# Kernel optimization log

Measured on AMD Instinct MI355X. Metric: run time of the kernel, lower is better.

## Reference

```python
import jax, jax.numpy as jnp
import numpy as np

B, L, H, O, NL = 1024, 100, 256, 256, 2


def setup_inputs() -> dict:
    key = jax.random.key(0)
    ks = jax.random.split(key, 20)
    s = 0.05  # weight scale to keep gates/softmax well-conditioned
    d = {
        "encoder_outputs": jax.random.normal(ks[0], (B, L, H), jnp.float32),
        "enc_h": jax.random.normal(ks[1], (NL, B, H), jnp.float32),
        "enc_c": jax.random.normal(ks[2], (NL, B, H), jnp.float32),
        "embedding": jax.random.uniform(ks[3], (O, H), jnp.float32, -1.0, 1.0),
        # torch nn.LSTM params, gate order (i, f, g, o)
        "Wih0": jax.random.normal(ks[4], (4 * H, 2 * H), jnp.float32) * s,
        "Whh0": jax.random.normal(ks[5], (4 * H, H), jnp.float32) * s,
        "bih0": jax.random.normal(ks[6], (4 * H,), jnp.float32) * s,
        "bhh0": jax.random.normal(ks[7], (4 * H,), jnp.float32) * s,
        "Wih1": jax.random.normal(ks[8], (4 * H, H), jnp.float32) * s,
        "Whh1": jax.random.normal(ks[9], (4 * H, H), jnp.float32) * s,
        "bih1": jax.random.normal(ks[10], (4 * H,), jnp.float32) * s,
        "bhh1": jax.random.normal(ks[11], (4 * H,), jnp.float32) * s,
        "Wa": jax.random.normal(ks[12], (H, H), jnp.float32) * s,        # Luong general score
        "Wconcat": jax.random.normal(ks[13], (H, 2 * H), jnp.float32) * s,
        "Wout": jax.random.normal(ks[14], (O, H), jnp.float32) * s,
        "Wcrit": jax.random.normal(ks[15], (O, O), jnp.float32) * s,
        "bcrit": jax.random.normal(ks[16], (O,), jnp.float32) * s,
        "actions": jax.random.randint(ks[17], (B, L), 0, O, jnp.int32),
    }
    return d


def _lstm_cell(x, h, c, Wih, Whh, bih, bhh):
    gates = x @ Wih.T + h @ Whh.T + bih + bhh  # [B, 4H]
    i, f, g, o = jnp.split(gates, 4, axis=-1)
    i = jax.nn.sigmoid(i)
    f = jax.nn.sigmoid(f)
    g = jnp.tanh(g)
    o = jax.nn.sigmoid(o)
    c_new = f * c + i * g
    h_new = o * jnp.tanh(c_new)
    return h_new, c_new


def reference(encoder_outputs, enc_h, enc_c, embedding,
              Wih0, Whh0, bih0, bhh0, Wih1, Whh1, bih1, bhh1,
              Wa, Wconcat, Wout, Wcrit, bcrit, actions):
    # Precompute Luong 'general' projection of encoder states (same math each step)
    enc_proj = encoder_outputs @ Wa.T  # [B, L, H]

    def step(carry, act_t):
        x, h, c, ctx = carry  # x:[B] int, h/c:[NL,B,H], ctx:[B,H]
        emb = embedding[x]                               # [B, H]
        inp = jnp.concatenate([emb, ctx], axis=-1)       # [B, 2H]
        h0, c0 = _lstm_cell(inp, h[0], c[0], Wih0, Whh0, bih0, bhh0)
        h1, c1 = _lstm_cell(h0, h[1], c[1], Wih1, Whh1, bih1, bhh1)
        out = h1                                         # [B, H]
        scores = jnp.einsum('bh,blh->bl', out, enc_proj)  # Luong general score
        attn = jax.nn.softmax(scores, axis=-1)
        ctx_att = jnp.einsum('bl,blh->bh', attn, encoder_outputs)
        new_ctx = jnp.tanh(jnp.concatenate([out, ctx_att], axis=-1) @ Wconcat.T)  # [B, H]
        logit_raw = new_ctx @ Wout.T                     # [B, O]
        pi = jax.nn.softmax(logit_raw, axis=-1)
        Q = logit_raw @ Wcrit.T + bcrit
        new_carry = (act_t, jnp.stack([h0, h1]), jnp.stack([c0, c1]), new_ctx)
        return new_carry, (pi, Q)

    x0 = jnp.zeros((B,), jnp.int32)
    ctx0 = encoder_outputs.mean(axis=1)                  # [B, H]
    _, (pis, Qs) = jax.lax.scan(step, (x0, enc_h, enc_c, ctx0), actions.T)
    logits = jnp.transpose(pis, (1, 0, 2))               # [B, L, O] (softmax probs, as in torch code)
    qvalues = jnp.transpose(Qs, (1, 0, 2))               # [B, L, O]
    values = (qvalues * logits).sum(-1)                  # [B, L]
    decoder_action = actions.astype(jnp.float32)         # teacher-forced actions recorded per step
    return decoder_action, logits, values
```

## Files before the change

### kernel.cpp

```cpp
#include <hip/hip_runtime.h>


#define Bx 1024
#define Lq 100
#define Hd 256
#define Od 256
#define H4 1024

typedef _Float16 f16;
typedef _Float16 half2_t __attribute__((ext_vector_type(2)));
typedef _Float16 f16x4 __attribute__((ext_vector_type(4)));
typedef unsigned int uint;
typedef uint uint4v __attribute__((ext_vector_type(4)));

__device__ __forceinline__ float fdot2(half2_t a, half2_t b, float c) {
#if __has_builtin(__builtin_amdgcn_fdot2)
  return __builtin_amdgcn_fdot2(a, b, c, false);
#else
  return c + (float)a.x * (float)b.x + (float)a.y * (float)b.y;
#endif
}
__device__ __forceinline__ float dot8(float acc, float4 w, float4 a) {
  acc = fdot2(__builtin_bit_cast(half2_t, w.x), __builtin_bit_cast(half2_t, a.x), acc);
  acc = fdot2(__builtin_bit_cast(half2_t, w.y), __builtin_bit_cast(half2_t, a.y), acc);
  acc = fdot2(__builtin_bit_cast(half2_t, w.z), __builtin_bit_cast(half2_t, a.z), acc);
  acc = fdot2(__builtin_bit_cast(half2_t, w.w), __builtin_bit_cast(half2_t, a.w), acc);
  return acc;
}
__device__ __forceinline__ float sigmf(float x) { return 1.0f / (1.0f + __expf(-x)); }



__global__ void k_cvt_lstm(const float* Wih0, const float* Whh0,
                           const float* Wih1, const float* Whh1, f16* dst) {
  int row = blockIdx.x, seg = row >> 10, r = row & 1023, c = threadIdx.x;
  const float* src; int stride, off;
  if (seg == 0)      { src = Wih0; stride = 512; off = 256; }
  else if (seg == 1) { src = Whh0; stride = 256; off = 0; }
  else if (seg == 2) { src = Wih1; stride = 256; off = 0; }
  else               { src = Whh1; stride = 256; off = 0; }
  size_t didx = (size_t)seg * 262144 + (size_t)(r >> 6) * 16384 +
                (size_t)(c >> 3) * 512 + (size_t)(r & 63) * 8 + (c & 7);
  dst[didx] = (f16)src[(size_t)r * stride + off + c];
}

__global__ void k_cvt_small(const float* Wconcat, const float* Wout,
                            const float* Wcrit, const float* Wa, f16* dst) {
  int blk = blockIdx.x, seg = blk >> 8, r = blk & 255, c = threadIdx.x;
  if (seg == 0) {
    dst[(size_t)(r >> 6) * 32768 + (size_t)(c >> 3) * 512 + (r & 63) * 8 + (c & 7)] =
        (f16)Wconcat[(size_t)r * 512 + c];
    int c2 = c + 256;
    dst[(size_t)(r >> 6) * 32768 + (size_t)(c2 >> 3) * 512 + (r & 63) * 8 + (c2 & 7)] =
        (f16)Wconcat[(size_t)r * 512 + c2];
  } else if (seg == 1) {
    dst[131072 + (size_t)(r >> 6) * 16384 + (size_t)(c >> 3) * 512 + (r & 63) * 8 + (c & 7)] =
        (f16)Wout[(size_t)r * 256 + c];
  } else if (seg == 2) {
    dst[196608 + (size_t)(r >> 6) * 16384 + (size_t)(c >> 3) * 512 + (r & 63) * 8 + (c & 7)] =
        (f16)Wcrit[(size_t)r * 256 + c];
  } else {
    dst[262144 + (size_t)(c >> 6) * 16384 + (size_t)(r >> 3) * 512 + (c & 63) * 8 + (r & 7)] =
        (f16)Wa[(size_t)r * 256 + c];
  }
}

__global__ void k_bias1(const float* bih1, const float* bhh1, float* b1) {
  int i = blockIdx.x * 256 + threadIdx.x;
  b1[i] = bih1[i] + bhh1[i];
}

__global__ void k_actions(const int* actions, float* out) {
  int i = blockIdx.x * 256 + threadIdx.x;
  out[i] = (float)actions[i];
}

__global__ void k_cvt_enc(const float* enc, f16* dst) {
  size_t i = (size_t)blockIdx.x * 256 + threadIdx.x;
  const float4* s = (const float4*)enc;
  float4 v = s[i];
  f16x4 o = {(f16)v.x, (f16)v.y, (f16)v.z, (f16)v.w};
  *(f16x4*)(dst + 4 * i) = o;
}

__global__ void k_table0(const float* emb, const float* Wih0,
                         const float* bih0, const float* bhh0, float* t0) {
  __shared__ float shw[16][256];
  int j0 = blockIdx.x * 16, tid = threadIdx.x;
  for (int i = tid; i < 16 * 256; i += 256) {
    int r = i >> 8, c = i & 255;
    shw[r][c] = Wih0[(size_t)(j0 + r) * 512 + c];
  }
  __syncthreads();
  int a = tid;
  float acc[16];
#pragma unroll
  for (int r = 0; r < 16; r++) acc[r] = 0.f;
  for (int k = 0; k < 256; k++) {
    float e = emb[(size_t)a * 256 + k];
#pragma unroll
    for (int r = 0; r < 16; r++) acc[r] = fmaf(e, shw[r][k], acc[r]);
  }
#pragma unroll
  for (int r = 0; r < 16; r++)
    t0[(size_t)a * H4 + j0 + r] = acc[r] + bih0[j0 + r] + bhh0[j0 + r];
}

template <bool E16>
__launch_bounds__(1024)
__global__ void k_seq(const float* enc, const f16* enc16,
                      const float* enc_h, const float* enc_c,
                      const int* actions, const float* bcrit,
                      const f16* wWih0c, const f16* wWhh0,
                      const f16* wWih1, const f16* wWhh1,
                      const f16* wWconcat, const f16* wWout, const f16* wWcrit,
                      const f16* wWaT,
                      const float* table0, const float* bias1, float* out) {
  const int tid = threadIdx.x;
  const int b0 = blockIdx.x * 4;

  __shared__ _Float16 sh_h0[4][264];
  __shared__ _Float16 sh_h1[4][264];
  __shared__ _Float16 sh_ctx[4][264];
  __shared__ _Float16 sh_ca[4][264];
  __shared__ _Float16 sh_logit[4][264];
  __shared__ _Float16 sh_v[4][264];
  __shared__ float sh_c0[4][256];
  __shared__ float sh_c1[4][256];
  __shared__ float sh_gates[4][H4];
  __shared__ float sh_sc[4][128];
  __shared__ float sh_pi[4][256];
  __shared__ float sh_red[4][20];

  {
    int bb = tid >> 8, h = tid & 255, gb = b0 + bb;
    sh_h0[bb][h] = (f16)enc_h[(size_t)(0 * Bx + gb) * Hd + h];
    sh_h1[bb][h] = (f16)enc_h[(size_t)(1 * Bx + gb) * Hd + h];
    sh_c0[bb][h] = enc_c[(size_t)(0 * Bx + gb) * Hd + h];
    sh_c1[bb][h] = enc_c[(size_t)(1 * Bx + gb) * Hd + h];
    const float* ep = enc + (size_t)gb * Lq * Hd + h;
    float s = 0.f;
#pragma unroll 4
    for (int l = 0; l < Lq; l++) s += __builtin_nontemporal_load(ep + (size_t)l * Hd);
    sh_ctx[bb][h] = (f16)(s * (1.0f / Lq));
  }
  __syncthreads();

  for (int t = 0; t < Lq; t++) {
    {
      const int j = tid;
      const f16* w1 = wWih0c + (size_t)(j >> 6) * 16384 + (j & 63) * 8;
      const f16* w2 = wWhh0 + (size_t)(j >> 6) * 16384 + (j & 63) * 8;
      int ia0 = (t == 0) ? 0 : actions[(size_t)(b0 + 0) * Lq + (t - 1)];
      int ia1 = (t == 0) ? 0 : actions[(size_t)(b0 + 1) * Lq + (t - 1)];
      int ia2 = (t == 0) ? 0 : actions[(size_t)(b0 + 2) * Lq + (t - 1)];
      int ia3 = (t == 0) ? 0 : actions[(size_t)(b0 + 3) * Lq + (t - 1)];
      float a0 = table0[(size_t)ia0 * H4 + j];
      float a1 = table0[(size_t)ia1 * H4 + j];
      float a2 = table0[(size_t)ia2 * H4 + j];
      float a3 = table0[(size_t)ia3 * H4 + j];
#pragma unroll 4
      for (int c = 0; c < 32; c++) {
        float4 wa = *(const float4*)(w1 + (size_t)c * 512);
        float4 wb = *(const float4*)(w2 + (size_t)c * 512);
        float4 x0 = *(const float4*)&sh_ctx[0][8 * c];
        float4 x1 = *(const float4*)&sh_ctx[1][8 * c];
        float4 x2 = *(const float4*)&sh_ctx[2][8 * c];
        float4 x3 = *(const float4*)&sh_ctx[3][8 * c];
        a0 = dot8(a0, wa, x0); a1 = dot8(a1, wa, x1);
        a2 = dot8(a2, wa, x2); a3 = dot8(a3, wa, x3);
        float4 y0 = *(const float4*)&sh_h0[0][8 * c];
        float4 y1 = *(const float4*)&sh_h0[1][8 * c];
        float4 y2 = *(const float4*)&sh_h0[2][8 * c];
        float4 y3 = *(const float4*)&sh_h0[3][8 * c];
        a0 = dot8(a0, wb, y0); a1 = dot8(a1, wb, y1);
        a2 = dot8(a2, wb, y2); a3 = dot8(a3, wb, y3);
      }
      sh_gates[0][j] = a0; sh_gates[1][j] = a1;
      sh_gates[2][j] = a2; sh_gates[3][j] = a3;
    }
    __syncthreads();

    {
      int bb = tid >> 8, h = tid & 255;
      float gi = sh_gates[bb][h], gf = sh_gates[bb][h + 256];
      float gg = sh_gates[bb][h + 512], go = sh_gates[bb][h + 768];
      float c = sigmf(gf) * sh_c0[bb][h] + sigmf(gi) * tanhf(gg);
      sh_c0[bb][h] = c;
      sh_h0[bb][h] = (f16)(sigmf(go) * tanhf(c));
    }
    __syncthreads();

    {
      const int j = tid;
      const f16* w1 = wWih1 + (size_t)(j >> 6) * 16384 + (j & 63) * 8;
      const f16* w2 = wWhh1 + (size_t)(j >> 6) * 16384 + (j & 63) * 8;
      float bv = bias1[j];
      float a0 = bv, a1 = bv, a2 = bv, a3 = bv;
#pragma unroll 4
      for (int c = 0; c < 32; c++) {
        float4 wa = *(const float4*)(w1 + (size_t)c * 512);
        float4 wb = *(const float4*)(w2 + (size_t)c * 512);
        float4 x0 = *(const float4*)&sh_h0[0][8 * c];
        float4 x1 = *(const float4*)&sh_h0[1][8 * c];
        float4 x2 = *(const float4*)&sh_h0[2][8 * c];
        float4 x3 = *(const float4*)&sh_h0[3][8 * c];
        a0 = dot8(a0, wa, x0); a1 = dot8(a1, wa, x1);
        a2 = dot8(a2, wa, x2); a3 = dot8(a3, wa, x3);
        float4 y0 = *(const float4*)&sh_h1[0][8 * c];
        float4 y1 = *(const float4*)&sh_h1[1][8 * c];
        float4 y2 = *(const float4*)&sh_h1[2][8 * c];
        float4 y3 = *(const float4*)&sh_h1[3][8 * c];
        a0 = dot8(a0, wb, y0); a1 = dot8(a1, wb, y1);
        a2 = dot8(a2, wb, y2); a3 = dot8(a3, wb, y3);
      }
      sh_gates[0][j] = a0; sh_gates[1][j] = a1;
      sh_gates[2][j] = a2; sh_gates[3][j] = a3;
    }
    __syncthreads();

    {
      int bb = tid >> 8, h = tid & 255;
      float gi = sh_gates[bb][h], gf = sh_gates[bb][h + 256];
      float gg = sh_gates[bb][h + 512], go = sh_gates[bb][h + 768];
      float c = sigmf(gf) * sh_c1[bb][h] + sigmf(gi) * tanhf(gg);
      sh_c1[bb][h] = c;
      sh_h1[bb][h] = (f16)(sigmf(go) * tanhf(c));
    }
    __syncthreads();

    {
      int bb = tid >> 8, h = tid & 255;
      const f16* w = wWaT + (size_t)(h >> 6) * 16384 + (h & 63) * 8;
      float s = 0.f;
#pragma unroll 4
      for (int c = 0; c < 32; c++) {
        float4 wv = *(const float4*)(w + (size_t)c * 512);
        float4 av = *(const float4*)&sh_h1[bb][8 * c];
        s = dot8(s, wv, av);
      }
      sh_v[bb][h] = (f16)s;
    }
    __syncthreads();

    {
      int bb = tid >> 8, r = tid & 255;
      int l = r & 127, kh = r >> 7;
      if (l < Lq) {
        if constexpr (E16) {
          const uint4v* ep =
              (const uint4v*)(enc16 + ((size_t)(b0 + bb) * Lq + l) * Hd) + kh * 16;
          float s = 0.f;
#pragma unroll 4
          for (int c = 0; c < 16; c++) {
            uint4v u = ep[c];
            float4 ev = __builtin_bit_cast(float4, u);
            float4 vv = *(const float4*)&sh_v[bb][8 * (kh * 16 + c)];
            s = dot8(s, ev, vv);
          }
          sh_gates[bb][kh * 128 + l] = s;
        } else {
          const float4* ep =
              (const float4*)(enc + ((size_t)(b0 + bb) * Lq + l) * Hd) + kh * 32;
          float s = 0.f;
#pragma unroll 4
          for (int c = 0; c < 32; c++) {
            float4 u = ep[c];
            const f16* vv = &sh_v[bb][4 * (kh * 32 + c)];
            s = fmaf(u.x, (float)vv[0], s);
            s = fmaf(u.y, (float)vv[1], s);
            s = fmaf(u.z, (float)vv[2], s);
            s = fmaf(u.w, (float)vv[3], s);
          }
          sh_gates[bb][kh * 128 + l] = s;
        }
      }
      __syncthreads();
      if (kh == 0 && l < Lq)
        sh_sc[bb][l] = sh_gates[bb][l] + sh_gates[bb][128 + l];
    }
    __syncthreads();

    if (tid < 256) {
      int bb = tid >> 6, lane = tid & 63;
      float v0 = (lane < Lq) ? sh_sc[bb][lane] : -1e30f;
      float v1 = (lane + 64 < Lq) ? sh_sc[bb][lane + 64] : -1e30f;
      float m = fmaxf(v0, v1);
      for (int off = 32; off; off >>= 1) m = fmaxf(m, __shfl_xor(m, off));
      float e0 = (lane < Lq) ? __expf(v0 - m) : 0.f;
      float e1 = (lane + 64 < Lq) ? __expf(v1 - m) : 0.f;
      float s = e0 + e1;
      for (int off = 32; off; off >>= 1) s += __shfl_xor(s, off);
      float inv = 1.0f / s;
      if (lane < Lq) sh_sc[bb][lane] = e0 * inv;
      if (lane + 64 < Lq) sh_sc[bb][lane + 64] = e1 * inv;
    }
    __syncthreads();

    if constexpr (E16) {
      int bb = tid >> 8, r = tid & 255;
      int hh = r & 127, half = r >> 7;
      const uint* ep = (const uint*)(enc16 + (size_t)(b0 + bb) * Lq * Hd) + hh;
      float s0 = 0.f, s1 = 0.f;
      int l0 = half * 50;
#pragma unroll 5
      for (int l = l0; l < l0 + 50; l++) {
        uint u = ep[(size_t)l * 128];
        half2_t hv = __builtin_bit_cast(half2_t, u);
        float a = sh_sc[bb][l];
        s0 = fmaf(a, (float)hv.x, s0);
        s1 = fmaf(a, (float)hv.y, s1);
      }
      sh_gates[bb][half * 512 + hh] = s0;
      sh_gates[bb][half * 512 + 128 + hh] = s1;
      __syncthreads();
      if (half == 0) {
        float r0 = sh_gates[bb][hh] + sh_gates[bb][512 + hh];
        float r1 = sh_gates[bb][128 + hh] + sh_gates[bb][512 + 128 + hh];
        half2_t rr = {(f16)r0, (f16)r1};
        *(half2_t*)&sh_ca[bb][2 * hh] = rr;
      }
    } else {
      int bb = tid >> 8, h = tid & 255;
      const float* ep = enc + (size_t)(b0 + bb) * Lq * Hd + h;
      float s = 0.f;
#pragma unroll 4
      for (int l = 0; l < Lq; l++)
        s = fmaf(sh_sc[bb][l], ep[(size_t)l * Hd], s);
      sh_ca[bb][h] = (f16)s;
    }
    __syncthreads();

    {
      int bb = tid >> 8, j = tid & 255;
      const f16* w = wWconcat + (size_t)(j >> 6) * 32768 + (j & 63) * 8;
      float s = 0.f;
#pragma unroll 4
      for (int c = 0; c < 32; c++) {
        float4 wv = *(const float4*)(w + (size_t)c * 512);
        float4 av = *(const float4*)&sh_h1[bb][8 * c];
        s = dot8(s, wv, av);
      }
#pragma unroll 4
      for (int c = 0; c < 32; c++) {
        float4 wv = *(const float4*)(w + (size_t)(32 + c) * 512);
        float4 av = *(const float4*)&sh_ca[bb][8 * c];
        s = dot8(s, wv, av);
      }
      sh_ctx[bb][j] = (f16)tanhf(s);
    }
    __syncthreads();

    {
      int bb = tid >> 8, o = tid & 255;
      const f16* w = wWout + (size_t)(o >> 6) * 16384 + (o & 63) * 8;
      float s = 0.f;
#pragma unroll 4
      for (int c = 0; c < 32; c++) {
        float4 wv = *(const float4*)(w + (size_t)c * 512);
        float4 av = *(const float4*)&sh_ctx[bb][8 * c];
        s = dot8(s, wv, av);
      }
      sh_logit[bb][o] = (f16)s;
      sh_pi[bb][o] = s;
    }
    __syncthreads();

    {
      int bb = tid >> 8, o = tid & 255, wv = (tid >> 6) & 3, lane = tid & 63;
      float v = sh_pi[bb][o];
      float e = __expf(v);
      float s = e;
      for (int off = 32; off; off >>= 1) s += __shfl_xor(s, off);
      if (lane == 0) sh_red[bb][4 + wv] = s;
      __syncthreads();
      s = sh_red[bb][4] + sh_red[bb][5] + sh_red[bb][6] + sh_red[bb][7];
      float pi = e * (1.0f / s);
      sh_pi[bb][o] = pi;
      out[(size_t)Bx * Lq + ((size_t)(b0 + bb) * Lq + t) * Od + o] = pi;
    }
    __syncthreads();

    {
      int bb = tid >> 8, o = tid & 255, wv = (tid >> 6) & 3, lane = tid & 63;
      const f16* w = wWcrit + (size_t)(o >> 6) * 16384 + (o & 63) * 8;
      float q = bcrit[o];
#pragma unroll 4
      for (int c = 0; c < 32; c++) {
        float4 wv4 = *(const float4*)(w + (size_t)c * 512);
        float4 lv = *(const float4*)&sh_logit[bb][8 * c];
        q = dot8(q, wv4, lv);
      }
      float pv = sh_pi[bb][o] * q;
      for (int off = 32; off; off >>= 1) pv += __shfl_xor(pv, off);
      if (lane == 0) sh_red[bb][8 + wv] = pv;
    }
    __syncthreads();
    if (tid < 4) {
      float v = sh_red[tid][8] + sh_red[tid][9] + sh_red[tid][10] + sh_red[tid][11];
      out[(size_t)Bx * Lq * (1 + Od) + (size_t)(b0 + tid) * Lq + t] = v;
    }
  }
}

extern "C" void kernel_launch(void* const* d_in, const int* in_sizes, int n_in,
                              void* d_out, int out_size, void* d_ws, size_t ws_size,
                              hipStream_t stream) {
  const float* enc    = (const float*)d_in[0];
  const float* enc_h  = (const float*)d_in[1];
  const float* enc_c  = (const float*)d_in[2];
  const float* emb    = (const float*)d_in[3];
  const float* Wih0   = (const float*)d_in[4];
  const float* Whh0   = (const float*)d_in[5];
  const float* bih0   = (const float*)d_in[6];
  const float* bhh0   = (const float*)d_in[7];
  const float* Wih1   = (const float*)d_in[8];
  const float* Whh1   = (const float*)d_in[9];
  const float* bih1   = (const float*)d_in[10];
  const float* bhh1   = (const float*)d_in[11];
  const float* Wa     = (const float*)d_in[12];
  const float* Wconcat= (const float*)d_in[13];
  const float* Wout   = (const float*)d_in[14];
  const float* Wcrit  = (const float*)d_in[15];
  const float* bcrit  = (const float*)d_in[16];
  const int* actions  = (const int*)d_in[17];
  float* out = (float*)d_out;

  const size_t ENC16_B = 52428800;
  const size_t W_B     = 2752512;
  const size_t T0_B    = 1048576;
  const size_t B1_B    = 4096;
  bool e16 = ws_size >= ENC16_B + W_B + T0_B + B1_B;

  char* ws = (char*)d_ws;
  f16* wsEnc16 = (f16*)ws;
  size_t base = e16 ? ENC16_B : 0;
  f16* wsW    = (f16*)(ws + base);
  float* wsT0 = (float*)(ws + base + W_B);
  float* wsB1 = (float*)(ws + base + W_B + T0_B);

  const f16* wWih0c   = wsW;
  const f16* wWhh0    = wsW + 262144;
  const f16* wWih1    = wsW + 524288;
  const f16* wWhh1    = wsW + 786432;
  const f16* wWconcat = wsW + 1048576;
  const f16* wWout    = wsW + 1179648;
  const f16* wWcrit   = wsW + 1245184;
  const f16* wWaT     = wsW + 1310720;

  hipLaunchKernelGGL(k_cvt_lstm, dim3(4096), dim3(256), 0, stream,
                     Wih0, Whh0, Wih1, Whh1, wsW);
  hipLaunchKernelGGL(k_cvt_small, dim3(1024), dim3(256), 0, stream,
                     Wconcat, Wout, Wcrit, Wa, (f16*)(wsW + 1048576));
  hipLaunchKernelGGL(k_bias1, dim3(4), dim3(256), 0, stream, bih1, bhh1, wsB1);
  hipLaunchKernelGGL(k_table0, dim3(64), dim3(256), 0, stream,
                     emb, Wih0, bih0, bhh0, wsT0);
  hipLaunchKernelGGL(k_actions, dim3(400), dim3(256), 0, stream, actions, out);
  if (e16) {
    hipLaunchKernelGGL(k_cvt_enc, dim3(25600), dim3(256), 0, stream, enc, wsEnc16);
    hipLaunchKernelGGL(k_seq<true>, dim3(256), dim3(1024), 0, stream,
                       enc, wsEnc16, enc_h, enc_c, actions, bcrit,
                       wWih0c, wWhh0, wWih1, wWhh1, wWconcat, wWout, wWcrit, wWaT,
                       wsT0, wsB1, out);
  } else {
    hipLaunchKernelGGL(k_seq<false>, dim3(256), dim3(1024), 0, stream,
                       enc, (const f16*)nullptr, enc_h, enc_c, actions, bcrit,
                       wWih0c, wWhh0, wWih1, wWhh1, wWconcat, wWout, wWcrit, wWaT,
                       wsT0, wsB1, out);
  }
}
```

Baseline: 6.380 ms.

## Fuse attention scores, softmax and context into single-pass streaming over encoder rows

Replaces the three-phase attention (score GEMV, separate softmax, weighted sum) with one pass in which each wavefront streams 25 encoder rows, computes each score with a wave-wide shuffle reduction, exponentiates it, and accumulates the unnormalized context and partial sum. The four partial results are then combined and divided by the total. This reads the encoder slice once per step instead of twice and removes several barriers. The softmax no longer subtracts the max, which risks overflow if scores are large, and it adds a six-level shuffle reduction per row.

Result: faster. 5.967 ms (-6.5%).

```diff
diff --git a/kernel.cpp b/kernel.cpp
--- a/kernel.cpp
+++ b/kernel.cpp
@@ -128,7 +128,8 @@
   __shared__ float sh_c0[4][256];
   __shared__ float sh_c1[4][256];
   __shared__ float sh_gates[4][H4];
-  __shared__ float sh_sc[4][128];
+  __shared__ float sh_accp[4][4][256];
+  __shared__ float sh_zz[4][4];
   __shared__ float sh_pi[4][256];
   __shared__ float sh_red[4][20];
 
@@ -244,90 +245,62 @@
     __syncthreads();
 
     {
-      int bb = tid >> 8, r = tid & 255;
-      int l = r & 127, kh = r >> 7;
-      if (l < Lq) {
-        if constexpr (E16) {
-          const uint4v* ep =
-              (const uint4v*)(enc16 + ((size_t)(b0 + bb) * Lq + l) * Hd) + kh * 16;
-          float s = 0.f;
-#pragma unroll 4
-          for (int c = 0; c < 16; c++) {
-            uint4v u = ep[c];
-            float4 ev = __builtin_bit_cast(float4, u);
-            float4 vv = *(const float4*)&sh_v[bb][8 * (kh * 16 + c)];
-            s = dot8(s, ev, vv);
-          }
-          sh_gates[bb][kh * 128 + l] = s;
-        } else {
-          const float4* ep =
-              (const float4*)(enc + ((size_t)(b0 + bb) * Lq + l) * Hd) + kh * 32;
-          float s = 0.f;
-#pragma unroll 4
-          for (int c = 0; c < 32; c++) {
-            float4 u = ep[c];
-            const f16* vv = &sh_v[bb][4 * (kh * 32 + c)];
-            s = fmaf(u.x, (float)vv[0], s);
-            s = fmaf(u.y, (float)vv[1], s);
-            s = fmaf(u.z, (float)vv[2], s);
-            s = fmaf(u.w, (float)vv[3], s);
-          }
-          sh_gates[bb][kh * 128 + l] = s;
+      const int w = tid >> 6, lane = tid & 63;
+      const int bb = w >> 2, q = w & 3;
+      float Z = 0.f, a0 = 0.f, a1 = 0.f, a2 = 0.f, a3 = 0.f;
+      if constexpr (E16) {
+        uint2 vv = *(const uint2*)&sh_v[bb][lane * 4];
+        const uint2* ep =
+            (const uint2*)(enc16 + ((size_t)(b0 + bb) * Lq + q * 25) * Hd) + lane;
+#pragma unroll 5
+        for (int l = 0; l < 25; l++) {
+          uint2 u = ep[(size_t)l * 64];
+          float s = fdot2(__builtin_bit_cast(half2_t, u.x),
+                          __builtin_bit_cast(half2_t, vv.x), 0.f);
+          s = fdot2(__builtin_bit_cast(half2_t, u.y),
+                    __builtin_bit_cast(half2_t, vv.y), s);
+          for (int off = 32; off; off >>= 1) s += __shfl_xor(s, off);
+          float p = __expf(s);
+          Z += p;
+          half2_t h01 = __builtin_bit_cast(half2_t, u.x);
+          half2_t h23 = __builtin_bit_cast(half2_t, u.y);
+          a0 = fmaf(p, (float)h01.x, a0);
+          a1 = fmaf(p, (float)h01.y, a1);
+          a2 = fmaf(p, (float)h23.x, a2);
+          a3 = fmaf(p, (float)h23.y, a3);
         }
-      }
-      __syncthreads();
-      if (kh == 0 && l < Lq)
-        sh_sc[bb][l] = sh_gates[bb][l] + sh_gates[bb][128 + l];
-    }
-    __syncthreads();
-
-    if (tid < 256) {
-      int bb = tid >> 6, lane = tid & 63;
-      float v0 = (lane < Lq) ? sh_sc[bb][lane] : -1e30f;
-      float v1 = (lane + 64 < Lq) ? sh_sc[bb][lane + 64] : -1e30f;
-      float m = fmaxf(v0, v1);
-      for (int off = 32; off; off >>= 1) m = fmaxf(m, __shfl_xor(m, off));
-      float e0 = (lane < Lq) ? __expf(v0 - m) : 0.f;
-      float e1 = (lane + 64 < Lq) ? __expf(v1 - m) : 0.f;
-      float s = e0 + e1;
-      for (int off = 32; off; off >>= 1) s += __shfl_xor(s, off);
-      float inv = 1.0f / s;
-      if (lane < Lq) sh_sc[bb][lane] = e0 * inv;
-      if (lane + 64 < Lq) sh_sc[bb][lane + 64] = e1 * inv;
-    }
-    __syncthreads();
-
-    if constexpr (E16) {
-      int bb = tid >> 8, r = tid & 255;
-      int hh = r & 127, half = r >> 7;
-      const uint* ep = (const uint*)(enc16 + (size_t)(b0 + bb) * Lq * Hd) + hh;
-      float s0 = 0.f, s1 = 0.f;
-      int l0 = half * 50;
+      } else {
+        float v0 = (float)sh_v[bb][lane * 4 + 0];
+        float v1 = (float)sh_v[bb][lane * 4 + 1];
+        float v2 = (float)sh_v[bb][lane * 4 + 2];
+        float v3 = (float)sh_v[bb][lane * 4 + 3];
+        const float4* ep =
+            (const float4*)(enc + ((size_t)(b0 + bb) * Lq + q * 25) * Hd) + lane;
 #pragma unroll 5
-      for (int l = l0; l < l0 + 50; l++) {
-        uint u = ep[(size_t)l * 128];
-        half2_t hv = __builtin_bit_cast(half2_t, u);
-        float a = sh_sc[bb][l];
-        s0 = fmaf(a, (float)hv.x, s0);
-        s1 = fmaf(a, (float)hv.y, s1);
-      }
-      sh_gates[bb][half * 512 + hh] = s0;
-      sh_gates[bb][half * 512 + 128 + hh] = s1;
-      __syncthreads();
-      if (half == 0) {
-        float r0 = sh_gates[bb][hh] + sh_gates[bb][512 + hh];
-        float r1 = sh_gates[bb][128 + hh] + sh_gates[bb][512 + 128 + hh];
-        half2_t rr = {(f16)r0, (f16)r1};
-        *(half2_t*)&sh_ca[bb][2 * hh] = rr;
-      }
-    } else {
+        for (int l = 0; l < 25; l++) {
+          float4 u = ep[(size_t)l * 64];
+          float s = u.x * v0 + u.y * v1 + u.z * v2 + u.w * v3;
+          for (int off = 32; off; off >>= 1) s += __shfl_xor(s, off);
+          float p = __expf(s);
+          Z += p;
+          a0 = fmaf(p, u.x, a0);
+          a1 = fmaf(p, u.y, a1);
+          a2 = fmaf(p, u.z, a2);
+          a3 = fmaf(p, u.w, a3);
+        }
+      }
+      float* ap = &sh_accp[bb][q][lane * 4];
+      ap[0] = a0; ap[1] = a1; ap[2] = a2; ap[3] = a3;
+      if (lane == 0) sh_zz[bb][q] = Z;
+    }
+    __syncthreads();
+
+    {
       int bb = tid >> 8, h = tid & 255;
-      const float* ep = enc + (size_t)(b0 + bb) * Lq * Hd + h;
-      float s = 0.f;
-#pragma unroll 4
-      for (int l = 0; l < Lq; l++)
-        s = fmaf(sh_sc[bb][l], ep[(size_t)l * Hd], s);
-      sh_ca[bb][h] = (f16)s;
+      float Zt = sh_zz[bb][0] + sh_zz[bb][1] + sh_zz[bb][2] + sh_zz[bb][3];
+      float c = sh_accp[bb][0][h] + sh_accp[bb][1][h] +
+                sh_accp[bb][2][h] + sh_accp[bb][3][h];
+      sh_ca[bb][h] = (f16)(c / Zt);
     }
     __syncthreads();
 
```
